# Kernel optimization log

Measured on AMD Instinct MI355X. Metric: run time of the kernel, lower is better.

Reference implementation:

```python
import jax, jax.numpy as jnp
import numpy as np

N = 21  # nodes per graph (20 laser sectors + 1 robot node)
MAX_RANGE = 10.0
_bound = np.linspace(-np.pi / 2 - 0.03, np.pi / 2, 21, dtype=np.float32)[:-1]
_angles = _bound + np.float32(np.pi / 20)
ANGLE_FEAT = jnp.asarray(np.stack([np.sin(_angles), np.cos(_angles)], 1), dtype=jnp.float32)  # [20,2]


def _build_nodes(state24):
    # state24: [B,24] -> node features [B,21,7]
    B = state24.shape[0]
    laser = state24[:, :20, None] / MAX_RANGE                       # [B,20,1]
    angle = jnp.broadcast_to(ANGLE_FEAT[None], (B, 20, 2))          # [B,20,2]
    sector = jnp.concatenate([laser, angle, jnp.zeros((B, 20, 4), state24.dtype)], -1)  # [B,20,7]
    robot = jnp.concatenate([jnp.zeros((B, 1, 3), state24.dtype), state24[:, None, 20:]], -1)  # [B,1,7]
    return jnp.concatenate([sector, robot], axis=1)                 # [B,21,7]


def _gatv2(x, Wl, Wr, att, bias, heads, dim):
    # GATv2 over a fully-connected graph with self-loops (dense all-pairs).
    # e_ij = att . leaky_relu(Wl x_j + Wr x_i); alpha = softmax_j; out_i = sum_j alpha_ij (Wl x_j)
    B = x.shape[0]
    gl = (x @ Wl).reshape(B, N, heads, dim)  # source transform [B,j,H,D]
    gr = (x @ Wr).reshape(B, N, heads, dim)  # target transform [B,i,H,D]
    s = jax.nn.leaky_relu(gl[:, None] + gr[:, :, None], negative_slope=0.2)  # [B,i,j,H,D]
    e = jnp.einsum('bijhd,hd->bijh', s, att)                                  # [B,i,j,H]
    alpha = jax.nn.softmax(e, axis=2)                                          # softmax over sources j
    out = jnp.einsum('bijh,bjhd->bihd', alpha, gl).reshape(B, N, heads * dim)
    return out + bias


def setup_inputs() -> dict:
    key = jax.random.key(0)
    ks = jax.random.split(key, 16)
    r = lambda k, shape, s: (jax.random.normal(k, shape, dtype=jnp.float32) * s)
    B = 1024
    return {
        'state24': jax.random.normal(ks[0], (B, 24), dtype=jnp.float32),
        'Wl1': r(ks[1], (7, 256), 0.3), 'Wr1': r(ks[2], (7, 256), 0.3),
        'att1': r(ks[3], (4, 64), 0.1), 'b1': r(ks[4], (256,), 0.02),
        'Wl2': r(ks[5], (256, 64), 0.06), 'Wr2': r(ks[6], (256, 64), 0.06),
        'att2': r(ks[7], (1, 64), 0.1), 'b2': r(ks[8], (64,), 0.02),
        'fc1_w': r(ks[9], (64, 256), 0.12), 'fc1_b': r(ks[10], (256,), 0.02),
        'fc2_w': r(ks[11], (256, 256), 0.06), 'fc2_b': r(ks[12], (256,), 0.02),
        'fc3_w': r(ks[13], (256, 2), 0.06), 'fc3_b': r(ks[14], (2,), 0.02),
    }


def reference(state24, Wl1, Wr1, att1, b1, Wl2, Wr2, att2, b2,
              fc1_w, fc1_b, fc2_w, fc2_b, fc3_w, fc3_b):
    x = _build_nodes(state24)                               # [B,21,7]
    h = jax.nn.elu(_gatv2(x, Wl1, Wr1, att1, b1, 4, 64))    # [B,21,256]
    h = _gatv2(h, Wl2, Wr2, att2, b2, 1, 64)                # [B,21,64]
    nfv = jnp.mean(h, axis=1)                               # global_mean_pool -> [B,64]
    h = jax.nn.relu(nfv @ fc1_w + fc1_b)
    h = jax.nn.relu(h @ fc2_w + fc2_b)
    return jnp.tanh(h @ fc3_w + fc3_b)                      # [B,2]
```

## Files before the change

### kernel.cpp

```cpp
#include <hip/hip_runtime.h>
#include <hip/hip_fp16.h>
#include <math.h>

#define PI_D 3.141592653589793

typedef _Float16 h2 __attribute__((ext_vector_type(2)));
typedef _Float16 h4 __attribute__((ext_vector_type(4)));
typedef _Float16 h8 __attribute__((ext_vector_type(8)));
typedef unsigned short us8 __attribute__((ext_vector_type(8)));
typedef __fp16 f16v2 __attribute__((ext_vector_type(2)));
typedef __fp16 f16v8 __attribute__((ext_vector_type(8)));
typedef float f32x4 __attribute__((ext_vector_type(4)));

#define STR1 264
#define STR2H 72

#define SV(v, a, b) __builtin_shufflevector(v, v, a, b)

static __device__ __forceinline__ h2 pack_h2(float a, float b) {
    return __builtin_bit_cast(h2, __builtin_amdgcn_cvt_pkrtz(a, b));
}

static __device__ __forceinline__ float fdot2(h2 a, h2 b, float c) {
    return __builtin_amdgcn_fdot2(__builtin_bit_cast(f16v2, a),
                                  __builtin_bit_cast(f16v2, b), c, false);
}

static __device__ __forceinline__ h8 habs8(h8 x) {
    us8 u = __builtin_bit_cast(us8, x);
    us8 m = {0x7fff, 0x7fff, 0x7fff, 0x7fff, 0x7fff, 0x7fff, 0x7fff, 0x7fff};
    return __builtin_bit_cast(h8, (us8)(u & m));
}

static __device__ __forceinline__ f32x4 mfma16(h8 a, h8 b, f32x4 c) {
    return __builtin_amdgcn_mfma_f32_16x16x32_f16(
        __builtin_bit_cast(f16v8, a), __builtin_bit_cast(f16v8, b), c, 0, 0, 0);
}

static __device__ __forceinline__ void wave_fence() {
    asm volatile("" ::: "memory");
#if __has_builtin(__builtin_amdgcn_wave_barrier)
    __builtin_amdgcn_wave_barrier();
#endif
    asm volatile("" ::: "memory");
}

__global__ __launch_bounds__(256) void pack_weights_kernel(
    const float* __restrict__ Wl2, const float* __restrict__ Wr2,
    const float* __restrict__ fc1_w, const float* __restrict__ fc2_w,
    h8* __restrict__ ws)
{
    int idx = blockIdx.x * 256 + threadIdx.x;
    if (idx < 4096) {
        const float* W = idx < 2048 ? Wl2 : Wr2;
        int t = idx & 2047;
        int ntile = t >> 9, rem = t & 511;
        int kchunk = rem >> 6, lane = rem & 63;
        int n = ntile * 16 + (lane & 15);
        int k0 = kchunk * 32 + (lane >> 4) * 8;
        h8 o;
        #pragma unroll
        for (int j = 0; j < 8; ++j) o[j] = (_Float16)W[(k0 + j) * 64 + n];
        ws[idx] = o;
    } else if (idx < 6144) {
        int t = idx - 4096;
        int k2 = t >> 6, c = t & 63;
        h8 o;
        #pragma unroll
        for (int q = 0; q < 4; ++q) {
            o[2 * q]     = (_Float16)fc1_w[(2 * k2) * 256 + 4 * c + q];
            o[2 * q + 1] = (_Float16)fc1_w[(2 * k2 + 1) * 256 + 4 * c + q];
        }
        ws[idx] = o;
    } else {
        int t = idx - 6144;
        int k2 = t >> 6, c = t & 63;
        h8 o;
        #pragma unroll
        for (int q = 0; q < 4; ++q) {
            o[2 * q]     = (_Float16)fc2_w[(2 * k2) * 256 + 4 * c + q];
            o[2 * q + 1] = (_Float16)fc2_w[(2 * k2 + 1) * 256 + 4 * c + q];
        }
        ws[idx] = o;
    }
}

__global__ __launch_bounds__(256, 4) void actor_fused_kernel(
    const float* __restrict__ state24,
    const float* __restrict__ Wl1, const float* __restrict__ Wr1,
    const float* __restrict__ att1, const float* __restrict__ b1,
    const float* __restrict__ att2, const float* __restrict__ b2,
    const float* __restrict__ fc1_b, const float* __restrict__ fc2_b,
    const float* __restrict__ fc3_w, const float* __restrict__ fc3_b,
    const h8* __restrict__ wsL, const h8* __restrict__ wsR,
    const h8* __restrict__ wsF1, const h8* __restrict__ wsF2,
    float* __restrict__ out, int B)
{
    const int smp = blockIdx.x;
    const int tid = threadIdx.x;

    __shared__ float sinL[20], cosL[20], laserL[20], robotL[4];
    __shared__ __align__(16) h2 attLh[128];
    __shared__ __align__(16) h2 att2Lh[32];
    __shared__ __align__(16) _Float16 gr1h[22 * STR1];
    __shared__ __align__(16) union {
        struct { _Float16 gl1h[22 * STR1];
                 float ePf[128 * 24];
                 float uv[168]; } p1;
        struct { _Float16 gl2h[21 * STR2H];
                 _Float16 gr2h[21 * STR2H];
                 _Float16 gl2hT[64 * 32];
                 float e2[32 * 24];
                 float u2v2[42];
                 float red[4][256];
                 _Float16 nfvh[64]; _Float16 hah[256]; _Float16 hbh[256]; } p2;
    } U;

    if (tid < 20) {
        double step = (PI_D + 0.03) / 20.0;
        float bound = (float)(-PI_D / 2.0 - 0.03 + (double)tid * step);
        float ang = bound + (float)(PI_D / 20.0);
        sinL[tid] = sinf(ang);
        cosL[tid] = cosf(ang);
        laserL[tid] = state24[smp * 24 + tid] * 0.1f;
    }
    if (tid >= 32 && tid < 36) {
        int q = tid - 32;
        robotL[q] = state24[smp * 24 + 20 + q];
    }
    if (tid < 128) {
        float2 ap = ((const float2*)att1)[tid];
        attLh[tid] = pack_h2(0.4f * ap.x, 0.4f * ap.y);
    }
    if (tid >= 128 && tid < 160) {
        float2 ap = ((const float2*)att2)[tid - 128];
        att2Lh[tid - 128] = pack_h2(0.4f * ap.x, 0.4f * ap.y);
    }
    __syncthreads();

    {
        const int h = tid >> 6;
        const int lane = tid & 63;

        {
            const int cp = lane & 31;
            const int half = lane >> 5;
            const int d2 = h * 32 + cp;
            float2 wl[7], wr[7];
            #pragma unroll
            for (int k = 0; k < 7; k++) {
                wl[k] = ((const float2*)Wl1)[k * 128 + d2];
                wr[k] = ((const float2*)Wr1)[k * 128 + d2];
            }
            if (half == 0) {
                h2 zz2 = {};
                ((h2*)(U.p1.gl1h + 21 * STR1))[d2] = zz2;
                ((h2*)(gr1h + 21 * STR1))[d2] = zz2;
            }
            const int base = half * 11;
            #pragma unroll
            for (int nn = 0; nn < 11; ++nn) {
                int node = base + nn;
                if (node < 21) {
                    float a0, a1, b0, b1v;
                    if (node < 20) {
                        float l = laserL[node], sv = sinL[node], c = cosL[node];
                        a0 = l * wl[0].x + sv * wl[1].x + c * wl[2].x;
                        a1 = l * wl[0].y + sv * wl[1].y + c * wl[2].y;
                        b0 = l * wr[0].x + sv * wr[1].x + c * wr[2].x;
                        b1v = l * wr[0].y + sv * wr[1].y + c * wr[2].y;
                    } else {
                        float r0 = robotL[0], r1 = robotL[1], r2 = robotL[2], r3 = robotL[3];
                        a0 = r0 * wl[3].x + r1 * wl[4].x + r2 * wl[5].x + r3 * wl[6].x;
                        a1 = r0 * wl[3].y + r1 * wl[4].y + r2 * wl[5].y + r3 * wl[6].y;
                        b0 = r0 * wr[3].x + r1 * wr[4].x + r2 * wr[5].x + r3 * wr[6].x;
                        b1v = r0 * wr[3].y + r1 * wr[4].y + r2 * wr[5].y + r3 * wr[6].y;
                    }
                    ((h2*)(U.p1.gl1h + node * STR1))[d2] = pack_h2(a0, a1);
                    ((h2*)(gr1h + node * STR1))[d2] = pack_h2(b0, b1v);
                }
            }
        }
        wave_fence();

        {
            h2 ar[32];
            #pragma unroll
            for (int q = 0; q < 32; ++q) ar[q] = attLh[h * 32 + q];

            const bool act = lane < 63;
            const int jn  = act ? lane % 21 : 0;
            const int seg = act ? lane / 21 : 0;

            const h8* gA8 = (const h8*)(U.p1.gl1h + jn * STR1 + h * 64);
            h8 gj[8];
            #pragma unroll
            for (int ch = 0; ch < 8; ++ch) gj[ch] = gA8[ch];

            if (act && seg == 0) {
                float l0 = 0.f, l1 = 0.f;
                #pragma unroll
                for (int ch = 0; ch < 8; ++ch) {
                    l0 = fdot2(SV(gj[ch], 0, 1), ar[ch * 4 + 0], l0);
                    l1 = fdot2(SV(gj[ch], 2, 3), ar[ch * 4 + 1], l1);
                    l0 = fdot2(SV(gj[ch], 4, 5), ar[ch * 4 + 2], l0);
                    l1 = fdot2(SV(gj[ch], 6, 7), ar[ch * 4 + 3], l1);
                }
                U.p1.uv[h * 21 + jn] = l0 + l1;
            }

            #pragma unroll
            for (int t = 0; t < 7; ++t) {
                const int i = seg * 7 + t;
                const h8* gB8 = (const h8*)(gr1h + i * STR1 + h * 64);
                float m0 = 0.f, m1 = 0.f;
                #pragma unroll
                for (int ch = 0; ch < 8; ++ch) {
                    h8 x = gj[ch] + gB8[ch];
                    h8 ax = habs8(x);
                    m0 = fdot2(SV(ax, 0, 1), ar[ch * 4 + 0], m0);
                    m1 = fdot2(SV(ax, 2, 3), ar[ch * 4 + 1], m1);
                    m0 = fdot2(SV(ax, 4, 5), ar[ch * 4 + 2], m0);
                    m1 = fdot2(SV(ax, 6, 7), ar[ch * 4 + 3], m1);
                }
                if (act) U.p1.ePf[(h * 32 + i) * 24 + jn] = m0 + m1;
            }

            if (lane < 21) {
                const h8* row8 = (const h8*)(gr1h + lane * STR1 + h * 64);
                float l0 = 0.f, l1 = 0.f;
                #pragma unroll
                for (int ch = 0; ch < 8; ++ch) {
                    h8 g = row8[ch];
                    l0 = fdot2(SV(g, 0, 1), ar[ch * 4 + 0], l0);
                    l1 = fdot2(SV(g, 2, 3), ar[ch * 4 + 1], l1);
                    l0 = fdot2(SV(g, 4, 5), ar[ch * 4 + 2], l0);
                    l1 = fdot2(SV(g, 6, 7), ar[ch * 4 + 3], l1);
                }
                U.p1.uv[84 + h * 21 + lane] = l0 + l1;
            }
        }
        wave_fence();

        if (lane < 21) {
            int i = lane;
            int r = h * 32 + i;
            float* row = U.p1.ePf + r * 24;
            const float* uu = U.p1.uv + h * 21;
            float vi = 1.5f * U.p1.uv[84 + h * 21 + i];
            float ebuf[21];
            float m = -1e30f;
            #pragma unroll
            for (int j = 0; j < 21; j++) {
                float e = row[j] + 1.5f * uu[j] + vi;
                ebuf[j] = e;
                m = fmaxf(m, e);
            }
            float sum = 0.f;
            #pragma unroll
            for (int j = 0; j < 21; j++) { float v = __expf(ebuf[j] - m); ebuf[j] = v; sum += v; }
            float rinv = 1.f / sum;
            h8* hp8 = (h8*)(U.p1.ePf) + r * 6;
            h8 o0, o1, o2;
            #pragma unroll
            for (int q = 0; q < 8; ++q) o0[q] = (_Float16)(ebuf[q] * rinv);
            #pragma unroll
            for (int q = 0; q < 8; ++q) o1[q] = (_Float16)(ebuf[8 + q] * rinv);
            #pragma unroll
            for (int q = 0; q < 5; ++q) o2[q] = (_Float16)(ebuf[16 + q] * rinv);
            o2[5] = (_Float16)0.f; o2[6] = (_Float16)0.f; o2[7] = (_Float16)0.f;
            h8 zz = {};
            hp8[0] = o0; hp8[1] = o1; hp8[2] = o2;
            hp8[3] = zz; hp8[4] = zz; hp8[5] = zz;
        }
        {
            h8 zz = {};
            for (int z = lane; z < 66; z += 64) {
                int rr = z / 6, slot = z - rr * 6;
                ((h8*)U.p1.ePf)[(h * 32 + 21 + rr) * 6 + slot] = zz;
            }
        }
        wave_fence();

        {
            const int mcol = lane & 15;
            const int quad = lane >> 4;
            const h8* Af = (const h8*)U.p1.ePf;
            h8 A0 = Af[(h * 32 + mcol) * 6 + quad];
            h8 A1 = Af[(h * 32 + 16 + mcol) * 6 + quad];
            int rowoff[8];
            #pragma unroll
            for (int jj = 0; jj < 8; ++jj) {
                int rr = quad * 8 + jj;
                rowoff[jj] = (rr > 21 ? 21 : rr) * STR1;
            }
            const int colbase = h * 64 + mcol;
            f32x4 z4 = {0.f, 0.f, 0.f, 0.f};
            #pragma unroll
            for (int t = 0; t < 4; ++t) {
                int col = colbase + t * 16;
                float bb = b1[col];
                h8 bv;
                #pragma unroll
                for (int jj = 0; jj < 8; ++jj) bv[jj] = U.p1.gl1h[rowoff[jj] + col];
                f32x4 d0 = mfma16(A0, bv, z4);
                f32x4 d1 = mfma16(A1, bv, z4);
                #pragma unroll
                for (int r = 0; r < 4; ++r) {
                    int n0 = quad * 4 + r;
                    float v = d0[r] + bb;
                    v = v > 0.f ? v : __expf(v) - 1.f;
                    gr1h[n0 * STR1 + col] = (_Float16)v;
                    int n1 = 16 + quad * 4 + r;
                    if (n1 < 21) {
                        float w2 = d1[r] + bb;
                        w2 = w2 > 0.f ? w2 : __expf(w2) - 1.f;
                        gr1h[n1 * STR1 + col] = (_Float16)w2;
                    }
                }
            }
        }
    }
    __syncthreads();

    {
        const int lane = tid & 63;
        const int w = tid >> 6;
        const int mrow = lane & 15;
        const int quad = lane >> 4;
        int rowA1 = 16 + mrow; if (rowA1 > 21) rowA1 = 21;
        const h8* bL = wsL + w * 512 + lane;
        const h8* bR = wsR + w * 512 + lane;
        f32x4 aL0 = {0.f, 0.f, 0.f, 0.f}, aL1 = {0.f, 0.f, 0.f, 0.f};
        f32x4 aR0 = {0.f, 0.f, 0.f, 0.f}, aR1 = {0.f, 0.f, 0.f, 0.f};
        #pragma unroll
        for (int kc = 0; kc < 8; ++kc) {
            h8 BL = bL[kc * 64];
            h8 BR = bR[kc * 64];
            h8 A0 = *(const h8*)(gr1h + mrow * STR1 + quad * 8 + kc * 32);
            h8 A1 = *(const h8*)(gr1h + rowA1 * STR1 + quad * 8 + kc * 32);
            aL0 = mfma16(A0, BL, aL0);
            aL1 = mfma16(A1, BL, aL1);
            aR0 = mfma16(A0, BR, aR0);
            aR1 = mfma16(A1, BR, aR1);
        }
        const int col = w * 16 + mrow;
        #pragma unroll
        for (int r = 0; r < 4; ++r) {
            int row0 = quad * 4 + r;
            U.p2.gl2h[row0 * STR2H + col] = (_Float16)aL0[r];
            U.p2.gr2h[row0 * STR2H + col] = (_Float16)aR0[r];
            int row1 = 16 + row0;
            if (row1 < 21) {
                U.p2.gl2h[row1 * STR2H + col] = (_Float16)aL1[r];
                U.p2.gr2h[row1 * STR2H + col] = (_Float16)aR1[r];
            }
        }
        h2 lo0 = pack_h2(aL0[0], aL0[1]);
        h2 hi0 = pack_h2(aL0[2], aL0[3]);
        h4 p0 = __builtin_shufflevector(lo0, hi0, 0, 1, 2, 3);
        *(h4*)(U.p2.gl2hT + col * 32 + quad * 4) = p0;
        h2 lo1 = pack_h2(aL1[0], aL1[1]);
        h2 hi1 = pack_h2(aL1[2], aL1[3]);
        h4 p1 = __builtin_shufflevector(lo1, hi1, 0, 1, 2, 3);
        *(h4*)(U.p2.gl2hT + col * 32 + 16 + quad * 4) = p1;
    }
    __syncthreads();

    {
        h2 ar2[32];
        #pragma unroll
        for (int q = 0; q < 32; ++q) ar2[q] = att2Lh[q];

        const bool act = tid < 252;
        const int t0 = act ? tid : 0;
        const int jn = t0 % 21;
        const int sg = t0 / 21;

        const h8* gA8 = (const h8*)(U.p2.gl2h + jn * STR2H);
        h8 gj[8];
        #pragma unroll
        for (int ch = 0; ch < 8; ++ch) gj[ch] = gA8[ch];

        if (act && sg == 0) {
            float l0 = 0.f, l1 = 0.f;
            #pragma unroll
            for (int ch = 0; ch < 8; ++ch) {
                l0 = fdot2(SV(gj[ch], 0, 1), ar2[ch * 4 + 0], l0);
                l1 = fdot2(SV(gj[ch], 2, 3), ar2[ch * 4 + 1], l1);
                l0 = fdot2(SV(gj[ch], 4, 5), ar2[ch * 4 + 2], l0);
                l1 = fdot2(SV(gj[ch], 6, 7), ar2[ch * 4 + 3], l1);
            }
            U.p2.u2v2[jn] = l0 + l1;
        }

        if (sg < 11) {
            #pragma unroll
            for (int tt = 0; tt < 2; ++tt) {
                const int i = sg * 2 + tt;
                const int ri = i < 21 ? i : 20;
                const h8* gB8 = (const h8*)(U.p2.gr2h + ri * STR2H);
                float m0 = 0.f, m1 = 0.f;
                #pragma unroll
                for (int ch = 0; ch < 8; ++ch) {
                    h8 x = gj[ch] + gB8[ch];
                    h8 ax = habs8(x);
                    m0 = fdot2(SV(ax, 0, 1), ar2[ch * 4 + 0], m0);
                    m1 = fdot2(SV(ax, 2, 3), ar2[ch * 4 + 1], m1);
                    m0 = fdot2(SV(ax, 4, 5), ar2[ch * 4 + 2], m0);
                    m1 = fdot2(SV(ax, 6, 7), ar2[ch * 4 + 3], m1);
                }
                if (act && i < 21) U.p2.e2[i * 24 + jn] = m0 + m1;
            }
        } else if (act) {
            const h8* row8 = (const h8*)(U.p2.gr2h + jn * STR2H);
            float l0 = 0.f, l1 = 0.f;
            #pragma unroll
            for (int ch = 0; ch < 8; ++ch) {
                h8 g = row8[ch];
                l0 = fdot2(SV(g, 0, 1), ar2[ch * 4 + 0], l0);
                l1 = fdot2(SV(g, 2, 3), ar2[ch * 4 + 1], l1);
                l0 = fdot2(SV(g, 4, 5), ar2[ch * 4 + 2], l0);
                l1 = fdot2(SV(g, 6, 7), ar2[ch * 4 + 3], l1);
            }
            U.p2.u2v2[21 + jn] = l0 + l1;
        }
    }
    __syncthreads();

    if (tid < 21) {
        int i = tid;
        float* row = U.p2.e2 + i * 24;
        const float* uu = U.p2.u2v2;
        float vi = 1.5f * U.p2.u2v2[21 + i];
        float ebuf[21];
        float m = -1e30f;
        #pragma unroll
        for (int j = 0; j < 21; j++) {
            float e = row[j] + 1.5f * uu[j] + vi;
            ebuf[j] = e;
            m = fmaxf(m, e);
        }
        float sum = 0.f;
        #pragma unroll
        for (int j = 0; j < 21; j++) { float v = __expf(ebuf[j] - m); ebuf[j] = v; sum += v; }
        float rinv = 1.f / sum;
        h8* hp8 = (h8*)(U.p2.e2) + i * 6;
        h8 o0, o1, o2;
        #pragma unroll
        for (int q = 0; q < 8; ++q) o0[q] = (_Float16)(ebuf[q] * rinv);
        #pragma unroll
        for (int q = 0; q < 8; ++q) o1[q] = (_Float16)(ebuf[8 + q] * rinv);
        #pragma unroll
        for (int q = 0; q < 5; ++q) o2[q] = (_Float16)(ebuf[16 + q] * rinv);
        o2[5] = (_Float16)0.f; o2[6] = (_Float16)0.f; o2[7] = (_Float16)0.f;
        h8 zz = {};
        hp8[0] = o0; hp8[1] = o1; hp8[2] = o2;
        hp8[3] = zz; hp8[4] = zz; hp8[5] = zz;
    } else if (tid < 87) {
        int z = tid - 21;
        int rr = z / 6, slot = z - rr * 6;
        h8 zz = {};
        ((h8*)U.p2.e2)[(21 + rr) * 6 + slot] = zz;
    }
    __syncthreads();

    {
        const int lane = tid & 63;
        const int w = tid >> 6;
        const int mcol = lane & 15;
        const int quad = lane >> 4;
        const int col = w * 16 + mcol;
        float bb = b2[col];
        f32x4 z4 = {0.f, 0.f, 0.f, 0.f};
        const h8* Af2 = (const h8*)U.p2.e2;
        h8 A0 = Af2[mcol * 6 + quad];
        h8 A1 = Af2[(16 + mcol) * 6 + quad];
        h8 bv = *(const h8*)(U.p2.gl2hT + col * 32 + quad * 8);
        f32x4 d0 = mfma16(A0, bv, z4);
        f32x4 d1 = mfma16(A1, bv, z4);
        float sum = (d0[0] + d0[1]) + (d0[2] + d0[3])
                  + (d1[0] + d1[1]) + (d1[2] + d1[3]);
        sum += __shfl_xor(sum, 16, 64);
        sum += __shfl_xor(sum, 32, 64);
        if (quad == 0) U.p2.nfvh[col] = (_Float16)(sum * (1.f / 21.f) + bb);
    }
    __syncthreads();

    {
        int c = tid & 63, g = tid >> 6;
        float4 acc = {0.f, 0.f, 0.f, 0.f};
        #pragma unroll
        for (int kk = 0; kk < 8; ++kk) {
            int k2 = g * 8 + kk;
            h8 w = wsF1[k2 * 64 + c];
            h2 x = ((const h2*)U.p2.nfvh)[k2];
            acc.x = fdot2(SV(w, 0, 1), x, acc.x);
            acc.y = fdot2(SV(w, 2, 3), x, acc.y);
            acc.z = fdot2(SV(w, 4, 5), x, acc.z);
            acc.w = fdot2(SV(w, 6, 7), x, acc.w);
        }
        ((float4*)U.p2.red[g])[c] = acc;
    }
    __syncthreads();
    {
        float bb = fc1_b[tid];
        float v = U.p2.red[0][tid] + U.p2.red[1][tid]
                + U.p2.red[2][tid] + U.p2.red[3][tid] + bb;
        U.p2.hah[tid] = (_Float16)fmaxf(v, 0.f);
    }
    __syncthreads();

    {
        int c = tid & 63, g = tid >> 6;
        const h8* ha = (const h8*)U.p2.hah;
        float4 acc = {0.f, 0.f, 0.f, 0.f};
#define FC2_STEP(q, p)                                                          \
        {                                                                       \
            int k2 = g * 32 + (q) * 4 + (p);                                    \
            h8 w = wsF2[k2 * 64 + c];                                           \
            h2 x = __builtin_shufflevector(xa, xa, 2 * (p), 2 * (p) + 1);       \
            acc.x = fdot2(SV(w, 0, 1), x, acc.x);                               \
            acc.y = fdot2(SV(w, 2, 3), x, acc.y);                               \
            acc.z = fdot2(SV(w, 4, 5), x, acc.z);                               \
            acc.w = fdot2(SV(w, 6, 7), x, acc.w);                               \
        }
        #pragma unroll
        for (int q = 0; q < 8; ++q) {
            h8 xa = ha[g * 8 + q];
            FC2_STEP(q, 0)
            FC2_STEP(q, 1)
            FC2_STEP(q, 2)
            FC2_STEP(q, 3)
        }
#undef FC2_STEP
        ((float4*)U.p2.red[g])[c] = acc;
    }
    __syncthreads();
    {
        float bb = fc2_b[tid];
        float v = U.p2.red[0][tid] + U.p2.red[1][tid]
                + U.p2.red[2][tid] + U.p2.red[3][tid] + bb;
        U.p2.hbh[tid] = (_Float16)fmaxf(v, 0.f);
    }
    __syncthreads();

    {
        int g = tid >> 6;
        if (g < 2) {
            int o = g;
            int l = tid & 63;
            float sum = 0.f;
            #pragma unroll
            for (int m = 0; m < 4; m++) {
                int k = l + 64 * m;
                sum = fmaf((float)U.p2.hbh[k], fc3_w[k * 2 + o], sum);
            }
            #pragma unroll
            for (int off = 32; off >= 1; off >>= 1) sum += __shfl_down(sum, off, 64);
            if (l == 0) out[smp * 2 + o] = tanhf(sum + fc3_b[o]);
        }
    }
}

extern "C" void kernel_launch(void* const* d_in, const int* in_sizes, int n_in,
                              void* d_out, int out_size, void* d_ws, size_t ws_size,
                              hipStream_t stream) {
    const float* state24 = (const float*)d_in[0];
    const float* Wl1 = (const float*)d_in[1];
    const float* Wr1 = (const float*)d_in[2];
    const float* att1 = (const float*)d_in[3];
    const float* b1 = (const float*)d_in[4];
    const float* Wl2 = (const float*)d_in[5];
    const float* Wr2 = (const float*)d_in[6];
    const float* att2 = (const float*)d_in[7];
    const float* b2 = (const float*)d_in[8];
    const float* fc1_w = (const float*)d_in[9];
    const float* fc1_b = (const float*)d_in[10];
    const float* fc2_w = (const float*)d_in[11];
    const float* fc2_b = (const float*)d_in[12];
    const float* fc3_w = (const float*)d_in[13];
    const float* fc3_b = (const float*)d_in[14];
    float* out = (float*)d_out;

    h8* ws = (h8*)d_ws;
    const h8* wsL = ws;
    const h8* wsR = ws + 2048;
    const h8* wsF1 = ws + 4096;
    const h8* wsF2 = ws + 6144;

    pack_weights_kernel<<<56, 256, 0, stream>>>(Wl2, Wr2, fc1_w, fc2_w, ws);

    int B = in_sizes[0] / 24;
    actor_fused_kernel<<<B, 256, 0, stream>>>(
        state24, Wl1, Wr1, att1, b1, att2, b2,
        fc1_b, fc2_b, fc3_w, fc3_b,
        wsL, wsR, wsF1, wsF2, out, B);
}
```

Baseline: 112.9 us.

## Split MLP head into batched MFMA kernel over 32 samples per block

The fused per-sample kernel is split in two. The GAT kernel now writes the pooled node features to a workspace buffer, and a new fc_kernel runs the three MLP layers for 32 samples per block. fc1 and fc2 now use MFMA 16x16 tiles, and their weights are repacked into MFMA B-operand layout. This amortizes the fc weight reads across samples instead of reloading all fc weights per sample with fdot2, and it frees shared memory in the GAT kernel. The cost is an extra kernel launch and a round trip of the features through global memory. The fc kernel reads nfv rows up to the next multiple of 32 without a bounds check, which goes past B when B is not a multiple of 32.

```diff
diff --git a/kernel.cpp b/kernel.cpp
--- a/kernel.cpp
+++ b/kernel.cpp
@@ -14,6 +14,7 @@
 
 #define STR1 264
 #define STR2H 72
+#define STRF 264
 
 #define SV(v, a, b) __builtin_shufflevector(v, v, a, b)
 
@@ -64,37 +65,34 @@
         ws[idx] = o;
     } else if (idx < 6144) {
         int t = idx - 4096;
-        int k2 = t >> 6, c = t & 63;
+        int nt = t >> 7, rem = t & 127;
+        int kc = rem >> 6, lane = rem & 63;
+        int n = nt * 16 + (lane & 15);
+        int k0 = kc * 32 + (lane >> 4) * 8;
         h8 o;
         #pragma unroll
-        for (int q = 0; q < 4; ++q) {
-            o[2 * q]     = (_Float16)fc1_w[(2 * k2) * 256 + 4 * c + q];
-            o[2 * q + 1] = (_Float16)fc1_w[(2 * k2 + 1) * 256 + 4 * c + q];
-        }
+        for (int j = 0; j < 8; ++j) o[j] = (_Float16)fc1_w[(k0 + j) * 256 + n];
         ws[idx] = o;
     } else {
         int t = idx - 6144;
-        int k2 = t >> 6, c = t & 63;
+        int nt = t >> 9, rem = t & 511;
+        int kc = rem >> 6, lane = rem & 63;
+        int n = nt * 16 + (lane & 15);
+        int k0 = kc * 32 + (lane >> 4) * 8;
         h8 o;
         #pragma unroll
-        for (int q = 0; q < 4; ++q) {
-            o[2 * q]     = (_Float16)fc2_w[(2 * k2) * 256 + 4 * c + q];
-            o[2 * q + 1] = (_Float16)fc2_w[(2 * k2 + 1) * 256 + 4 * c + q];
-        }
+        for (int j = 0; j < 8; ++j) o[j] = (_Float16)fc2_w[(k0 + j) * 256 + n];
         ws[idx] = o;
     }
 }
 
-__global__ __launch_bounds__(256, 4) void actor_fused_kernel(
+__global__ __launch_bounds__(256, 4) void gat_kernel(
     const float* __restrict__ state24,
     const float* __restrict__ Wl1, const float* __restrict__ Wr1,
     const float* __restrict__ att1, const float* __restrict__ b1,
     const float* __restrict__ att2, const float* __restrict__ b2,
-    const float* __restrict__ fc1_b, const float* __restrict__ fc2_b,
-    const float* __restrict__ fc3_w, const float* __restrict__ fc3_b,
     const h8* __restrict__ wsL, const h8* __restrict__ wsR,
-    const h8* __restrict__ wsF1, const h8* __restrict__ wsF2,
-    float* __restrict__ out, int B)
+    _Float16* __restrict__ nfv, int B)
 {
     const int smp = blockIdx.x;
     const int tid = threadIdx.x;
@@ -111,9 +109,7 @@
                  _Float16 gr2h[21 * STR2H];
                  _Float16 gl2hT[64 * 32];
                  float e2[32 * 24];
-                 float u2v2[42];
-                 float red[4][256];
-                 _Float16 nfvh[64]; _Float16 hah[256]; _Float16 hbh[256]; } p2;
+                 float u2v2[42]; } p2;
     } U;
 
     if (tid < 20) {
@@ -483,83 +479,110 @@
                   + (d1[0] + d1[1]) + (d1[2] + d1[3]);
         sum += __shfl_xor(sum, 16, 64);
         sum += __shfl_xor(sum, 32, 64);
-        if (quad == 0) U.p2.nfvh[col] = (_Float16)(sum * (1.f / 21.f) + bb);
+        if (quad == 0) nfv[smp * 64 + col] = (_Float16)(sum * (1.f / 21.f) + bb);
+    }
+}
+
+__global__ __launch_bounds__(256) void fc_kernel(
+    const float* __restrict__ fc1_b, const float* __restrict__ fc2_b,
+    const float* __restrict__ fc3_w, const float* __restrict__ fc3_b,
+    const h8* __restrict__ wsF1, const h8* __restrict__ wsF2,
+    const _Float16* __restrict__ nfv, float* __restrict__ out, int B)
+{
+    const int tid = threadIdx.x;
+    const int w = tid >> 6;
+    const int lane = tid & 63;
+    const int mrow = lane & 15;
+    const int kq = lane >> 4;
+    const int mcol = lane & 15;
+    const int m0 = blockIdx.x * 32;
+
+    __shared__ __align__(16) _Float16 hah2[32 * STRF];
+    __shared__ __align__(16) _Float16 hbh2[32 * STRF];
+    __shared__ float p3[32][8][2];
+
+    h8 a1[2][2];
+    #pragma unroll
+    for (int mt = 0; mt < 2; ++mt)
+        #pragma unroll
+        for (int kc = 0; kc < 2; ++kc)
+            a1[mt][kc] = *(const h8*)(nfv + (m0 + mt * 16 + mrow) * 64 + kc * 32 + kq * 8);
+
+    #pragma unroll
+    for (int j = 0; j < 4; ++j) {
+        const int nt = w * 4 + j;
+        f32x4 acc[2] = {{0.f, 0.f, 0.f, 0.f}, {0.f, 0.f, 0.f, 0.f}};
+        #pragma unroll
+        for (int kc = 0; kc < 2; ++kc) {
+            h8 bb = wsF1[nt * 128 + kc * 64 + lane];
+            acc[0] = mfma16(a1[0][kc], bb, acc[0]);
+            acc[1] = mfma16(a1[1][kc], bb, acc[1]);
+        }
+        const int n = nt * 16 + mcol;
+        float bias = fc1_b[n];
+        #pragma unroll
+        for (int mt = 0; mt < 2; ++mt)
+            #pragma unroll
+            for (int r = 0; r < 4; ++r) {
+                float v = acc[mt][r] + bias;
+                hah2[(mt * 16 + kq * 4 + r) * STRF + n] = (_Float16)fmaxf(v, 0.f);
+            }
+    }
+    __syncthreads();
+
+    h8 a2[2][8];
+    #pragma unroll
+    for (int mt = 0; mt < 2; ++mt)
+        #pragma unroll
+        for (int kc = 0; kc < 8; ++kc)
+            a2[mt][kc] = *(const h8*)(hah2 + (mt * 16 + mrow) * STRF + kc * 32 + kq * 8);
+
+    #pragma unroll
+    for (int j = 0; j < 4; ++j) {
+        const int nt = w * 4 + j;
+        f32x4 acc[2] = {{0.f, 0.f, 0.f, 0.f}, {0.f, 0.f, 0.f, 0.f}};
+        #pragma unroll
+        for (int kc = 0; kc < 8; ++kc) {
+            h8 bb = wsF2[nt * 512 + kc * 64 + lane];
+            acc[0] = mfma16(a2[0][kc], bb, acc[0]);
+            acc[1] = mfma16(a2[1][kc], bb, acc[1]);
+        }
+        const int n = nt * 16 + mcol;
+        float bias = fc2_b[n];
+        #pragma unroll
+        for (int mt = 0; mt < 2; ++mt)
+            #pragma unroll
+            for (int r = 0; r < 4; ++r) {
+                float v = acc[mt][r] + bias;
+                hbh2[(mt * 16 + kq * 4 + r) * STRF + n] = (_Float16)fmaxf(v, 0.f);
+            }
     }
     __syncthreads();
 
     {
-        int c = tid & 63, g = tid >> 6;
-        float4 acc = {0.f, 0.f, 0.f, 0.f};
-        #pragma unroll
-        for (int kk = 0; kk < 8; ++kk) {
-            int k2 = g * 8 + kk;
-            h8 w = wsF1[k2 * 64 + c];
-            h2 x = ((const h2*)U.p2.nfvh)[k2];
-            acc.x = fdot2(SV(w, 0, 1), x, acc.x);
-            acc.y = fdot2(SV(w, 2, 3), x, acc.y);
-            acc.z = fdot2(SV(w, 4, 5), x, acc.z);
-            acc.w = fdot2(SV(w, 6, 7), x, acc.w);
-        }
-        ((float4*)U.p2.red[g])[c] = acc;
-    }
-    __syncthreads();
-    {
-        float bb = fc1_b[tid];
-        float v = U.p2.red[0][tid] + U.p2.red[1][tid]
-                + U.p2.red[2][tid] + U.p2.red[3][tid] + bb;
-        U.p2.hah[tid] = (_Float16)fmaxf(v, 0.f);
-    }
-    __syncthreads();
-
-    {
-        int c = tid & 63, g = tid >> 6;
-        const h8* ha = (const h8*)U.p2.hah;
-        float4 acc = {0.f, 0.f, 0.f, 0.f};
-#define FC2_STEP(q, p)                                                          \
-        {                                                                       \
-            int k2 = g * 32 + (q) * 4 + (p);                                    \
-            h8 w = wsF2[k2 * 64 + c];                                           \
-            h2 x = __builtin_shufflevector(xa, xa, 2 * (p), 2 * (p) + 1);       \
-            acc.x = fdot2(SV(w, 0, 1), x, acc.x);                               \
-            acc.y = fdot2(SV(w, 2, 3), x, acc.y);                               \
-            acc.z = fdot2(SV(w, 4, 5), x, acc.z);                               \
-            acc.w = fdot2(SV(w, 6, 7), x, acc.w);                               \
-        }
-        #pragma unroll
-        for (int q = 0; q < 8; ++q) {
-            h8 xa = ha[g * 8 + q];
-            FC2_STEP(q, 0)
-            FC2_STEP(q, 1)
-            FC2_STEP(q, 2)
-            FC2_STEP(q, 3)
-        }
-#undef FC2_STEP
-        ((float4*)U.p2.red[g])[c] = acc;
-    }
-    __syncthreads();
-    {
-        float bb = fc2_b[tid];
-        float v = U.p2.red[0][tid] + U.p2.red[1][tid]
-                + U.p2.red[2][tid] + U.p2.red[3][tid] + bb;
-        U.p2.hbh[tid] = (_Float16)fmaxf(v, 0.f);
-    }
-    __syncthreads();
-
-    {
-        int g = tid >> 6;
-        if (g < 2) {
-            int o = g;
-            int l = tid & 63;
-            float sum = 0.f;
-            #pragma unroll
-            for (int m = 0; m < 4; m++) {
-                int k = l + 64 * m;
-                sum = fmaf((float)U.p2.hbh[k], fc3_w[k * 2 + o], sum);
-            }
-            #pragma unroll
-            for (int off = 32; off >= 1; off >>= 1) sum += __shfl_down(sum, off, 64);
-            if (l == 0) out[smp * 2 + o] = tanhf(sum + fc3_b[o]);
-        }
+        const int s = tid >> 3;
+        const int u = tid & 7;
+        const _Float16* hr = hbh2 + s * STRF + u * 32;
+        float s0 = 0.f, s1 = 0.f;
+        #pragma unroll
+        for (int kk = 0; kk < 32; ++kk) {
+            float x = (float)hr[kk];
+            int k = u * 32 + kk;
+            s0 = fmaf(x, fc3_w[k * 2 + 0], s0);
+            s1 = fmaf(x, fc3_w[k * 2 + 1], s1);
+        }
+        p3[s][u][0] = s0;
+        p3[s][u][1] = s1;
+    }
+    __syncthreads();
+    if (tid < 64) {
+        const int s = tid >> 1;
+        const int o = tid & 1;
+        float tot = 0.f;
+        #pragma unroll
+        for (int u = 0; u < 8; ++u) tot += p3[s][u][o];
+        const int m = m0 + s;
+        if (m < B) out[m * 2 + o] = tanhf(tot + fc3_b[o]);
     }
 }
 
@@ -588,12 +611,17 @@
     const h8* wsR = ws + 2048;
     const h8* wsF1 = ws + 4096;
     const h8* wsF2 = ws + 6144;
+    _Float16* nfv = (_Float16*)(ws + 14336);
 
     pack_weights_kernel<<<56, 256, 0, stream>>>(Wl2, Wr2, fc1_w, fc2_w, ws);
 
     int B = in_sizes[0] / 24;
-    actor_fused_kernel<<<B, 256, 0, stream>>>(
+    gat_kernel<<<B, 256, 0, stream>>>(
         state24, Wl1, Wr1, att1, b1, att2, b2,
-        fc1_b, fc2_b, fc3_w, fc3_b,
-        wsL, wsR, wsF1, wsF2, out, B);
-}
+        wsL, wsR, nfv, B);
+
+    int nfc = (B + 31) / 32;
+    fc_kernel<<<nfc, 256, 0, stream>>>(
+        fc1_b, fc2_b, fc3_w, fc3_b, wsF1, wsF2,
+        (const _Float16*)nfv, out, B);
+}
```

Result: slower. 124.8 us (+10.5%).
